# Optimization experiments

Measured on AMD Instinct MI355X. Metric: run time of the kernel, lower is better.

## Reference

```python
import jax, jax.numpy as jnp
import numpy as np

B, C, N = 16, 256, 2048
D = C // 8  # q/k channel dim = 32
EPS = 1e-5
NEG_SLOPE = 0.2


def _conv1x1(x, w, b):
    # x: [B,C,N], w: [O,C], b: [O] -> [B,O,N]
    return jnp.einsum('oc,bcn->bon', w, x) + b[None, :, None]


def _bn(y, gamma, beta):
    # BatchNorm1d training-mode: per-channel stats over (batch, length)
    m = y.mean(axis=(0, 2), keepdims=True)
    v = y.var(axis=(0, 2), keepdims=True)  # biased, matches torch normalization
    return (y - m) * jax.lax.rsqrt(v + EPS) * gamma[None, :, None] + beta[None, :, None]


def setup_inputs() -> dict:
    key = jax.random.key(0)
    ks = jax.random.split(key, 14)
    s_qk = 1.0 / np.sqrt(C)
    return {
        'x': jax.random.normal(ks[0], (B, C, N), dtype=jnp.float32),
        'q_w': jax.random.normal(ks[1], (D, C), dtype=jnp.float32) * s_qk,
        'q_b': jnp.zeros((D,), jnp.float32),
        'q_g': jnp.ones((D,), jnp.float32),
        'q_be': jnp.zeros((D,), jnp.float32),
        'k_w': jax.random.normal(ks[2], (D, C), dtype=jnp.float32) * s_qk,
        'k_b': jnp.zeros((D,), jnp.float32),
        'k_g': jnp.ones((D,), jnp.float32),
        'k_be': jnp.zeros((D,), jnp.float32),
        'v_w': jax.random.normal(ks[3], (C, C), dtype=jnp.float32) * s_qk,
        'v_b': jnp.zeros((C,), jnp.float32),
        'v_g': jnp.ones((C,), jnp.float32),
        'v_be': jnp.zeros((C,), jnp.float32),
    }


def reference(x, q_w, q_b, q_g, q_be, k_w, k_b, k_g, k_be, v_w, v_b, v_g, v_be):
    # q, k: conv1x1 -> BN (no activation); v: conv1x1 -> BN -> LeakyReLU(0.2)
    q = _bn(_conv1x1(x, q_w, q_b), q_g, q_be)          # [B,D,N]
    k = _bn(_conv1x1(x, k_w, k_b), k_g, k_be)          # [B,D,N]
    v = jax.nn.leaky_relu(_bn(_conv1x1(x, v_w, v_b), v_g, v_be), NEG_SLOPE)  # [B,C,N]
    energy = jnp.einsum('bdn,bdm->bnm', q, k)          # [B,N,N]
    attn = jax.nn.softmax(energy, axis=-1)
    o = jnp.einsum('bcm,bnm->bcn', v, attn)            # attn applied over points
    return o + x
```

## Files before the change

kernel.cpp:

```cpp
#include <hip/hip_runtime.h>

#define BATCH 16
#define CH    256
#define NPT   2048
#define DQK   32
#define OTOT  320
#define EPSB  1e-5f
#define SLOPE 0.2f

typedef __attribute__((ext_vector_type(8))) short bf16x8;
typedef __attribute__((ext_vector_type(4))) float f32x4;

__device__ __forceinline__ unsigned short f2bf(float f) {
    unsigned u = __float_as_uint(f);
    u = (u + 0x7FFFu + ((u >> 16) & 1u)) >> 16;
    return (unsigned short)u;
}
__device__ __forceinline__ float bf2f(unsigned short h) {
    return __uint_as_float(((unsigned)h) << 16);
}

__global__ __launch_bounds__(256) void conv_kernel(
    const float* __restrict__ x,
    const float* __restrict__ qw, const float* __restrict__ qb,
    const float* __restrict__ kw, const float* __restrict__ kb,
    const float* __restrict__ vw, const float* __restrict__ vb,
    unsigned short* __restrict__ Ybf)
{
    int n  = blockIdx.x * 256 + threadIdx.x;
    int o0 = blockIdx.y * 16;
    int b  = blockIdx.z;

    const float* wsrc; const float* bsrc; int oo;
    if (o0 < 32)      { wsrc = qw; bsrc = qb; oo = o0;      }
    else if (o0 < 64) { wsrc = kw; bsrc = kb; oo = o0 - 32; }
    else              { wsrc = vw; bsrc = vb; oo = o0 - 64; }
    const float* w0 = wsrc + (size_t)oo * CH;

    const float* xb = x + (size_t)b * CH * NPT + n;
    float a[16];
#pragma unroll
    for (int j = 0; j < 16; ++j) a[j] = 0.f;

#pragma unroll 4
    for (int c = 0; c < CH; ++c) {
        float xv = xb[(size_t)c * NPT];
#pragma unroll
        for (int j = 0; j < 16; ++j)
            a[j] = fmaf(w0[j * CH + c], xv, a[j]);
    }
    unsigned short* yb = Ybf + ((size_t)b * OTOT + o0) * NPT + n;
#pragma unroll
    for (int j = 0; j < 16; ++j)
        yb[(size_t)j * NPT] = f2bf(a[j] + bsrc[oo + j]);
}

__global__ __launch_bounds__(256) void stats_kernel(
    const unsigned short* __restrict__ Ybf,
    const float* __restrict__ qg, const float* __restrict__ qbe,
    const float* __restrict__ kg, const float* __restrict__ kbe,
    const float* __restrict__ vg, const float* __restrict__ vbe,
    float* __restrict__ A, float* __restrict__ Cc)
{
    int o = blockIdx.x;
    float s = 0.f, ss = 0.f;
    for (int t = threadIdx.x; t < (BATCH * NPT) / 4; t += 256) {
        int b = t >> 9, n4 = (t & 511) * 4;
        const ushort4 v4 = *(const ushort4*)(Ybf + ((size_t)b * OTOT + o) * NPT + n4);
        float f0 = bf2f(v4.x), f1 = bf2f(v4.y), f2 = bf2f(v4.z), f3 = bf2f(v4.w);
        s  += f0 + f1 + f2 + f3;
        ss += f0*f0 + f1*f1 + f2*f2 + f3*f3;
    }
#pragma unroll
    for (int off = 32; off; off >>= 1) {
        s  += __shfl_down(s, off);
        ss += __shfl_down(ss, off);
    }
    __shared__ float ls[4], lss[4];
    int w = threadIdx.x >> 6, lane = threadIdx.x & 63;
    if (lane == 0) { ls[w] = s; lss[w] = ss; }
    __syncthreads();
    if (threadIdx.x == 0) {
        float S  = ls[0] + ls[1] + ls[2] + ls[3];
        float SS = lss[0] + lss[1] + lss[2] + lss[3];
        const float inv = 1.0f / (BATCH * NPT);
        float mean = S * inv;
        float var  = SS * inv - mean * mean;
        float g, be;
        if (o < 32)      { g = qg[o];      be = qbe[o];      }
        else if (o < 64) { g = kg[o - 32]; be = kbe[o - 32]; }
        else             { g = vg[o - 64]; be = vbe[o - 64]; }
        float a = g * rsqrtf(var + EPSB);
        A[o]  = a;
        Cc[o] = be - mean * a;
    }
}

__global__ __launch_bounds__(256) void normv_kernel(
    const unsigned short* __restrict__ Ybf,
    const float* __restrict__ A, const float* __restrict__ Cc,
    unsigned short* __restrict__ Vbf)
{
    size_t e = ((size_t)blockIdx.x * 256 + threadIdx.x) * 4;
    int b = (int)(e >> 19);
    int r = (int)(e & ((1u << 19) - 1));
    int c = r >> 11, n = r & (NPT - 1);
    const ushort4 v4 = *(const ushort4*)(Ybf + ((size_t)b * OTOT + 64 + c) * NPT + n);
    float a = A[64 + c], cc = Cc[64 + c];
    float f[4] = { bf2f(v4.x), bf2f(v4.y), bf2f(v4.z), bf2f(v4.w) };
    ushort4 o4;
    unsigned short* po = (unsigned short*)&o4;
#pragma unroll
    for (int i = 0; i < 4; ++i) {
        float y = f[i] * a + cc;
        y = (y > 0.f) ? y : SLOPE * y;
        po[i] = f2bf(y);
    }
    *(ushort4*)(Vbf + ((size_t)b * CH + c) * NPT + n) = o4;
}

__global__ __launch_bounds__(256) void transpose_qk_kernel(
    const unsigned short* __restrict__ Ybf,
    const float* __restrict__ A, const float* __restrict__ Cc,
    unsigned short* __restrict__ QKt)
{
    __shared__ unsigned short T[64][72];
    int b = blockIdx.y, n0 = blockIdx.x * 64;
    for (int e = threadIdx.x; e < 4096; e += 256) {
        int o = e >> 6, nn = e & 63;
        float y = bf2f(Ybf[((size_t)b * OTOT + o) * NPT + n0 + nn]);
        T[nn][o] = f2bf(y * A[o] + Cc[o]);
    }
    __syncthreads();
    for (int e = threadIdx.x; e < 4096; e += 256) {
        int nn = e >> 6, o = e & 63;
        QKt[((size_t)b * NPT + n0 + nn) * 64 + o] = T[nn][o];
    }
}

__global__ __launch_bounds__(256, 4) void attn_kernel(
    const unsigned short* __restrict__ QKt,
    const unsigned short* __restrict__ Vbf,
    const float* __restrict__ x,
    float* __restrict__ out)
{
    int L = blockIdx.x;
    int xcd = L & 7, k = L >> 3;
    int gi = k >> 5, n0i = k & 31;
    int grp = xcd * 4 + gi;
    int b = grp >> 1, z = grp & 1;
    int n0 = n0i * 64;

    int tid = threadIdx.x;
    int w = tid >> 6, lane = tid & 63;
    int quad = lane >> 4, l16 = lane & 15;

    const unsigned short* QK = QKt + (size_t)b * NPT * 64;
    const unsigned short* V  = Vbf + ((size_t)b * CH + z * 128) * NPT;

    __shared__ unsigned short Pbf[64][72];
    __shared__ float rsw[4][64];
    __shared__ float rtot[64];

    bf16x8 qa[4];
#pragma unroll
    for (int nt = 0; nt < 4; ++nt)
        qa[nt] = *(const bf16x8*)(QK + ((size_t)(n0 + nt * 16 + l16)) * 64 + quad * 8);

    f32x4 acc[4][2];
#pragma unroll
    for (int nt = 0; nt < 4; ++nt)
#pragma unroll
        for (int ct = 0; ct < 2; ++ct)
            acc[nt][ct] = (f32x4){0.f, 0.f, 0.f, 0.f};

    float rsum[4][4];
#pragma unroll
    for (int nt = 0; nt < 4; ++nt)
#pragma unroll
        for (int r = 0; r < 4; ++r) rsum[nt][r] = 0.f;

    const f32x4 zero4 = (f32x4){0.f, 0.f, 0.f, 0.f};

    for (int mt = 0; mt < NPT / 64; ++mt) {
        bf16x8 kb = *(const bf16x8*)(QK + ((size_t)(mt * 64 + w * 16 + l16)) * 64 + 32 + quad * 8);

        __syncthreads();

#pragma unroll
        for (int nt = 0; nt < 4; ++nt) {
            f32x4 s = __builtin_amdgcn_mfma_f32_16x16x32_bf16(qa[nt], kb, zero4, 0, 0, 0);
#pragma unroll
            for (int r = 0; r < 4; ++r) {
                float p = __expf(s[r]);
                rsum[nt][r] += p;
                Pbf[nt * 16 + quad * 4 + r][w * 16 + l16] = f2bf(p);
            }
        }
        __syncthreads();

#pragma unroll
        for (int ks = 0; ks < 2; ++ks) {
            bf16x8 pa[4];
#pragma unroll
            for (int nt = 0; nt < 4; ++nt)
                pa[nt] = *(const bf16x8*)&Pbf[nt * 16 + l16][ks * 32 + quad * 8];
#pragma unroll
            for (int ct = 0; ct < 2; ++ct) {
                const unsigned short* vp =
                    V + ((size_t)(w * 32 + ct * 16 + l16)) * NPT + mt * 64 + ks * 32 + quad * 8;
                bf16x8 vb = *(const bf16x8*)vp;
#pragma unroll
                for (int nt = 0; nt < 4; ++nt)
                    acc[nt][ct] = __builtin_amdgcn_mfma_f32_16x16x32_bf16(pa[nt], vb, acc[nt][ct], 0, 0, 0);
            }
        }
    }

#pragma unroll
    for (int nt = 0; nt < 4; ++nt)
#pragma unroll
        for (int r = 0; r < 4; ++r) {
            float v = rsum[nt][r];
            v += __shfl_xor(v, 1);
            v += __shfl_xor(v, 2);
            v += __shfl_xor(v, 4);
            v += __shfl_xor(v, 8);
            if (l16 == 0) rsw[w][nt * 16 + quad * 4 + r] = v;
        }
    __syncthreads();
    if (tid < 64)
        rtot[tid] = 1.0f / (rsw[0][tid] + rsw[1][tid] + rsw[2][tid] + rsw[3][tid]);
    __syncthreads();

    float rin[4][4];
#pragma unroll
    for (int nt = 0; nt < 4; ++nt)
#pragma unroll
        for (int r = 0; r < 4; ++r) rin[nt][r] = rtot[nt * 16 + quad * 4 + r];

#pragma unroll
    for (int nt = 0; nt < 4; ++nt)
#pragma unroll
        for (int ct = 0; ct < 2; ++ct) {
            int c = z * 128 + w * 32 + ct * 16 + l16;
            int n = n0 + nt * 16 + quad * 4;
            size_t gi4 = ((size_t)b * CH + c) * NPT + n;
            float4 xv = *(const float4*)(x + gi4);
            float4 o;
            o.x = acc[nt][ct][0] * rin[nt][0] + xv.x;
            o.y = acc[nt][ct][1] * rin[nt][1] + xv.y;
            o.z = acc[nt][ct][2] * rin[nt][2] + xv.z;
            o.w = acc[nt][ct][3] * rin[nt][3] + xv.w;
            *(float4*)(out + gi4) = o;
        }
}

extern "C" void kernel_launch(void* const* d_in, const int* in_sizes, int n_in,
                              void* d_out, int out_size, void* d_ws, size_t ws_size,
                              hipStream_t stream)
{
    const float* x   = (const float*)d_in[0];
    const float* qw  = (const float*)d_in[1];
    const float* qb  = (const float*)d_in[2];
    const float* qg  = (const float*)d_in[3];
    const float* qbe = (const float*)d_in[4];
    const float* kw  = (const float*)d_in[5];
    const float* kb  = (const float*)d_in[6];
    const float* kg  = (const float*)d_in[7];
    const float* kbe = (const float*)d_in[8];
    const float* vw  = (const float*)d_in[9];
    const float* vb  = (const float*)d_in[10];
    const float* vg  = (const float*)d_in[11];
    const float* vbe = (const float*)d_in[12];
    float* out = (float*)d_out;

    unsigned short* Ybf = (unsigned short*)d_ws;
    unsigned short* QKt = Ybf + (size_t)BATCH * OTOT * NPT;
    unsigned short* Vbf = QKt + (size_t)BATCH * NPT * 64;
    float* A  = (float*)(Vbf + (size_t)BATCH * CH * NPT);
    float* Cc = A + OTOT;

    conv_kernel <<<dim3(NPT / 256, OTOT / 16, BATCH), 256, 0, stream>>>(x, qw, qb, kw, kb, vw, vb, Ybf);
    stats_kernel<<<OTOT, 256, 0, stream>>>(Ybf, qg, qbe, kg, kbe, vg, vbe, A, Cc);
    normv_kernel<<<(BATCH * CH * NPT) / 1024, 256, 0, stream>>>(Ybf, A, Cc, Vbf);
    transpose_qk_kernel<<<dim3(NPT / 64, BATCH), 256, 0, stream>>>(Ybf, A, Cc, QKt);
    attn_kernel <<<1024, 256, 0, stream>>>(QKt, Vbf, x, out);
}
```

Baseline: 301.5 us.

## Fuse BN statistics into conv epilogue and merge V-normalize with QK transpose

Moves the BatchNorm sum and sum-of-squares into the conv kernel epilogue using wave reductions plus atomics, so Ybf no longer has to be re-read by a separate stats pass. A small finalize kernel then computes the scale and shift. The conv now uses pre-transposed weights for contiguous loads and computes 4 points per thread with float4 loads. The V-normalize and QK-transpose kernels are merged into one pack kernel with vectorized accesses. In exchange, the conv grid shrinks to 2x20x16 blocks, which may cut parallelism. Atomic float adds also make the statistics summation order nondeterministic.

New measurement: 315.4 us. 1.05x slower.

```diff
diff --git a/kernel.cpp b/kernel.cpp
--- a/kernel.cpp
+++ b/kernel.cpp
@@ -20,121 +20,144 @@
     return __uint_as_float(((unsigned)h) << 16);
 }
 
-__global__ __launch_bounds__(256) void conv_kernel(
-    const float* __restrict__ x,
+__global__ __launch_bounds__(256) void prep_kernel(
     const float* __restrict__ qw, const float* __restrict__ qb,
     const float* __restrict__ kw, const float* __restrict__ kb,
     const float* __restrict__ vw, const float* __restrict__ vb,
-    unsigned short* __restrict__ Ybf)
-{
-    int n  = blockIdx.x * 256 + threadIdx.x;
+    float* __restrict__ Wt, float* __restrict__ Bv)
+{
+    int idx = blockIdx.x * 256 + threadIdx.x;
+    int o = idx >> 8, c = idx & 255;
+    float w;
+    if (o < 32)      w = qw[(size_t)o * CH + c];
+    else if (o < 64) w = kw[(size_t)(o - 32) * CH + c];
+    else             w = vw[(size_t)(o - 64) * CH + c];
+    Wt[(size_t)c * OTOT + o] = w;
+    if (idx < OTOT) {
+        int oo = idx;
+        float bb;
+        if (oo < 32)      bb = qb[oo];
+        else if (oo < 64) bb = kb[oo - 32];
+        else              bb = vb[oo - 64];
+        Bv[oo] = bb;
+    }
+}
+
+__global__ __launch_bounds__(256) void conv_kernel(
+    const float* __restrict__ x,
+    const float* __restrict__ Wt, const float* __restrict__ Bv,
+    unsigned short* __restrict__ Ybf,
+    float* __restrict__ Sum, float* __restrict__ Sq)
+{
+    int nh = blockIdx.x;
     int o0 = blockIdx.y * 16;
     int b  = blockIdx.z;
-
-    const float* wsrc; const float* bsrc; int oo;
-    if (o0 < 32)      { wsrc = qw; bsrc = qb; oo = o0;      }
-    else if (o0 < 64) { wsrc = kw; bsrc = kb; oo = o0 - 32; }
-    else              { wsrc = vw; bsrc = vb; oo = o0 - 64; }
-    const float* w0 = wsrc + (size_t)oo * CH;
+    int n  = nh * 1024 + threadIdx.x * 4;
 
     const float* xb = x + (size_t)b * CH * NPT + n;
-    float a[16];
-#pragma unroll
-    for (int j = 0; j < 16; ++j) a[j] = 0.f;
-
-#pragma unroll 4
+
+    float4 acc[16];
+#pragma unroll
+    for (int j = 0; j < 16; ++j) acc[j] = make_float4(0.f, 0.f, 0.f, 0.f);
+
+#pragma unroll 2
     for (int c = 0; c < CH; ++c) {
-        float xv = xb[(size_t)c * NPT];
-#pragma unroll
-        for (int j = 0; j < 16; ++j)
-            a[j] = fmaf(w0[j * CH + c], xv, a[j]);
-    }
+        float4 xv = *(const float4*)(xb + (size_t)c * NPT);
+        const float* wr = Wt + (size_t)c * OTOT + o0;
+#pragma unroll
+        for (int j = 0; j < 16; ++j) {
+            float w = wr[j];
+            acc[j].x = fmaf(w, xv.x, acc[j].x);
+            acc[j].y = fmaf(w, xv.y, acc[j].y);
+            acc[j].z = fmaf(w, xv.z, acc[j].z);
+            acc[j].w = fmaf(w, xv.w, acc[j].w);
+        }
+    }
+
     unsigned short* yb = Ybf + ((size_t)b * OTOT + o0) * NPT + n;
-#pragma unroll
-    for (int j = 0; j < 16; ++j)
-        yb[(size_t)j * NPT] = f2bf(a[j] + bsrc[oo + j]);
-}
-
-__global__ __launch_bounds__(256) void stats_kernel(
-    const unsigned short* __restrict__ Ybf,
+    int lane = threadIdx.x & 63;
+#pragma unroll
+    for (int j = 0; j < 16; ++j) {
+        float bias = Bv[o0 + j];
+        float v0 = acc[j].x + bias, v1 = acc[j].y + bias;
+        float v2 = acc[j].z + bias, v3 = acc[j].w + bias;
+        ushort4 o4;
+        o4.x = f2bf(v0); o4.y = f2bf(v1); o4.z = f2bf(v2); o4.w = f2bf(v3);
+        *(ushort4*)(yb + (size_t)j * NPT) = o4;
+        float s  = v0 + v1 + v2 + v3;
+        float ss = v0*v0 + v1*v1 + v2*v2 + v3*v3;
+#pragma unroll
+        for (int off = 32; off; off >>= 1) {
+            s  += __shfl_down(s, off);
+            ss += __shfl_down(ss, off);
+        }
+        if (lane == 0) {
+            atomicAdd(&Sum[o0 + j], s);
+            atomicAdd(&Sq[o0 + j], ss);
+        }
+    }
+}
+
+__global__ __launch_bounds__(320) void finalize_kernel(
+    const float* __restrict__ Sum, const float* __restrict__ Sq,
     const float* __restrict__ qg, const float* __restrict__ qbe,
     const float* __restrict__ kg, const float* __restrict__ kbe,
     const float* __restrict__ vg, const float* __restrict__ vbe,
     float* __restrict__ A, float* __restrict__ Cc)
 {
-    int o = blockIdx.x;
-    float s = 0.f, ss = 0.f;
-    for (int t = threadIdx.x; t < (BATCH * NPT) / 4; t += 256) {
-        int b = t >> 9, n4 = (t & 511) * 4;
-        const ushort4 v4 = *(const ushort4*)(Ybf + ((size_t)b * OTOT + o) * NPT + n4);
-        float f0 = bf2f(v4.x), f1 = bf2f(v4.y), f2 = bf2f(v4.z), f3 = bf2f(v4.w);
-        s  += f0 + f1 + f2 + f3;
-        ss += f0*f0 + f1*f1 + f2*f2 + f3*f3;
-    }
-#pragma unroll
-    for (int off = 32; off; off >>= 1) {
-        s  += __shfl_down(s, off);
-        ss += __shfl_down(ss, off);
-    }
-    __shared__ float ls[4], lss[4];
-    int w = threadIdx.x >> 6, lane = threadIdx.x & 63;
-    if (lane == 0) { ls[w] = s; lss[w] = ss; }
-    __syncthreads();
-    if (threadIdx.x == 0) {
-        float S  = ls[0] + ls[1] + ls[2] + ls[3];
-        float SS = lss[0] + lss[1] + lss[2] + lss[3];
-        const float inv = 1.0f / (BATCH * NPT);
-        float mean = S * inv;
-        float var  = SS * inv - mean * mean;
-        float g, be;
-        if (o < 32)      { g = qg[o];      be = qbe[o];      }
-        else if (o < 64) { g = kg[o - 32]; be = kbe[o - 32]; }
-        else             { g = vg[o - 64]; be = vbe[o - 64]; }
-        float a = g * rsqrtf(var + EPSB);
-        A[o]  = a;
-        Cc[o] = be - mean * a;
-    }
-}
-
-__global__ __launch_bounds__(256) void normv_kernel(
+    int o = threadIdx.x;
+    if (o >= OTOT) return;
+    const float inv = 1.0f / (BATCH * NPT);
+    float mean = Sum[o] * inv;
+    float var  = Sq[o] * inv - mean * mean;
+    float g, be;
+    if (o < 32)      { g = qg[o];      be = qbe[o];      }
+    else if (o < 64) { g = kg[o - 32]; be = kbe[o - 32]; }
+    else             { g = vg[o - 64]; be = vbe[o - 64]; }
+    float a = g * rsqrtf(var + EPSB);
+    A[o]  = a;
+    Cc[o] = be - mean * a;
+}
+
+__global__ __launch_bounds__(256) void pack_kernel(
     const unsigned short* __restrict__ Ybf,
     const float* __restrict__ A, const float* __restrict__ Cc,
-    unsigned short* __restrict__ Vbf)
-{
-    size_t e = ((size_t)blockIdx.x * 256 + threadIdx.x) * 4;
-    int b = (int)(e >> 19);
-    int r = (int)(e & ((1u << 19) - 1));
-    int c = r >> 11, n = r & (NPT - 1);
-    const ushort4 v4 = *(const ushort4*)(Ybf + ((size_t)b * OTOT + 64 + c) * NPT + n);
-    float a = A[64 + c], cc = Cc[64 + c];
-    float f[4] = { bf2f(v4.x), bf2f(v4.y), bf2f(v4.z), bf2f(v4.w) };
-    ushort4 o4;
-    unsigned short* po = (unsigned short*)&o4;
-#pragma unroll
-    for (int i = 0; i < 4; ++i) {
-        float y = f[i] * a + cc;
-        y = (y > 0.f) ? y : SLOPE * y;
-        po[i] = f2bf(y);
-    }
-    *(ushort4*)(Vbf + ((size_t)b * CH + c) * NPT + n) = o4;
-}
-
-__global__ __launch_bounds__(256) void transpose_qk_kernel(
-    const unsigned short* __restrict__ Ybf,
-    const float* __restrict__ A, const float* __restrict__ Cc,
-    unsigned short* __restrict__ QKt)
-{
+    unsigned short* __restrict__ QKt, unsigned short* __restrict__ Vbf)
+{
+    int b = blockIdx.y, n0 = blockIdx.x * 64;
+    int tid = threadIdx.x;
+
+    for (int e = tid; e < 4096; e += 256) {
+        int c = e >> 4, n4 = (e & 15) * 4;
+        ushort4 v4 = *(const ushort4*)(Ybf + ((size_t)b * OTOT + 64 + c) * NPT + n0 + n4);
+        float a = A[64 + c], cc = Cc[64 + c];
+        ushort4 w4;
+        unsigned short* pi = (unsigned short*)&v4;
+        unsigned short* po = (unsigned short*)&w4;
+#pragma unroll
+        for (int i = 0; i < 4; ++i) {
+            float y = bf2f(pi[i]) * a + cc;
+            y = (y > 0.f) ? y : SLOPE * y;
+            po[i] = f2bf(y);
+        }
+        *(ushort4*)(Vbf + ((size_t)b * CH + c) * NPT + n0 + n4) = w4;
+    }
+
     __shared__ unsigned short T[64][72];
-    int b = blockIdx.y, n0 = blockIdx.x * 64;
-    for (int e = threadIdx.x; e < 4096; e += 256) {
-        int o = e >> 6, nn = e & 63;
-        float y = bf2f(Ybf[((size_t)b * OTOT + o) * NPT + n0 + nn]);
-        T[nn][o] = f2bf(y * A[o] + Cc[o]);
+    for (int e = tid; e < 1024; e += 256) {
+        int o = e >> 4, n4 = (e & 15) * 4;
+        ushort4 v4 = *(const ushort4*)(Ybf + ((size_t)b * OTOT + o) * NPT + n0 + n4);
+        float a = A[o], cc = Cc[o];
+        unsigned short* pi = (unsigned short*)&v4;
+#pragma unroll
+        for (int i = 0; i < 4; ++i)
+            T[n4 + i][o] = f2bf(bf2f(pi[i]) * a + cc);
     }
     __syncthreads();
-    for (int e = threadIdx.x; e < 4096; e += 256) {
-        int nn = e >> 6, o = e & 63;
-        QKt[((size_t)b * NPT + n0 + nn) * 64 + o] = T[nn][o];
+    for (int e = tid; e < 1024; e += 256) {
+        int nn = e >> 4, o4 = (e & 15) * 4;
+        ushort4 v4 = *(const ushort4*)&T[nn][o4];
+        *(ushort4*)(QKt + ((size_t)b * NPT + n0 + nn) * 64 + o4) = v4;
     }
 }
 
@@ -278,12 +301,18 @@
     unsigned short* Ybf = (unsigned short*)d_ws;
     unsigned short* QKt = Ybf + (size_t)BATCH * OTOT * NPT;
     unsigned short* Vbf = QKt + (size_t)BATCH * NPT * 64;
-    float* A  = (float*)(Vbf + (size_t)BATCH * CH * NPT);
-    float* Cc = A + OTOT;
-
-    conv_kernel <<<dim3(NPT / 256, OTOT / 16, BATCH), 256, 0, stream>>>(x, qw, qb, kw, kb, vw, vb, Ybf);
-    stats_kernel<<<OTOT, 256, 0, stream>>>(Ybf, qg, qbe, kg, kbe, vg, vbe, A, Cc);
-    normv_kernel<<<(BATCH * CH * NPT) / 1024, 256, 0, stream>>>(Ybf, A, Cc, Vbf);
-    transpose_qk_kernel<<<dim3(NPT / 64, BATCH), 256, 0, stream>>>(Ybf, A, Cc, QKt);
-    attn_kernel <<<1024, 256, 0, stream>>>(QKt, Vbf, x, out);
-}
+    float* tail = (float*)(Vbf + (size_t)BATCH * CH * NPT);
+    float* Sum = tail;
+    float* Sq  = tail + OTOT;
+    float* A   = tail + 2 * OTOT;
+    float* Cc  = tail + 3 * OTOT;
+    float* Wt = (float*)QKt;
+    float* Bv = Wt + (size_t)CH * OTOT;
+
+    hipMemsetAsync(Sum, 0, 2 * OTOT * sizeof(float), stream);
+    prep_kernel    <<<320, 256, 0, stream>>>(qw, qb, kw, kb, vw, vb, Wt, Bv);
+    conv_kernel    <<<dim3(2, OTOT / 16, BATCH), 256, 0, stream>>>(x, Wt, Bv, Ybf, Sum, Sq);
+    finalize_kernel<<<1, 320, 0, stream>>>(Sum, Sq, qg, qbe, kg, kbe, vg, vbe, A, Cc);
+    pack_kernel    <<<dim3(NPT / 64, BATCH), 256, 0, stream>>>(Ybf, A, Cc, QKt, Vbf);
+    attn_kernel    <<<1024, 256, 0, stream>>>(QKt, Vbf, x, out);
+}
```
